# Optimization experiments

Measured on AMD Instinct MI355X. Metric: run time of the kernel, lower is better.

Reference implementation:

```python
import jax, jax.numpy as jnp
import numpy as np


def setup_inputs() -> dict:
    key = jax.random.key(0)
    ks = jax.random.split(key, 10)
    B, D_X, D_H, D_S, D_T = 16384, 256, 512, 128, 128
    G = 4 * D_H
    sc = lambda d: 1.0 / np.sqrt(d)
    return {
        "x": jax.random.normal(ks[0], (B, D_X), jnp.float32),
        "h": jax.random.normal(ks[1], (B, D_H), jnp.float32),
        "c": jax.random.normal(ks[2], (B, D_H), jnp.float32),
        "spatial_per_step": jax.random.normal(ks[3], (B, D_S), jnp.float32),
        "temporal_per_step": jax.random.normal(ks[4], (B, D_T), jnp.float32),
        "W_x": jax.random.normal(ks[5], (D_X, G), jnp.float32) * sc(D_X),
        "W_h": jax.random.normal(ks[6], (D_H, G), jnp.float32) * sc(D_H),
        "b_h": jax.random.normal(ks[7], (G,), jnp.float32) * 0.01,
        "W_s": jax.random.normal(ks[8], (D_S, G), jnp.float32) * sc(D_S),
        "W_t": jax.random.normal(ks[9], (D_T, G), jnp.float32) * sc(D_T),
    }


def reference(x, h, c, spatial_per_step, temporal_per_step, W_x, W_h, b_h, W_s, W_t):
    H = W_h.shape[0]  # hidden_size
    # Four gate projections summed (the fusion opportunity): [B, 4H]
    preact = (x @ W_x) + (h @ W_h + b_h) + (spatial_per_step @ W_s) + (temporal_per_step @ W_t)
    i_g = jax.nn.sigmoid(preact[:, 0 * H:1 * H])
    f_g = jax.nn.sigmoid(preact[:, 1 * H:2 * H])
    o_g = jax.nn.sigmoid(preact[:, 2 * H:3 * H])
    c_g = jnp.tanh(preact[:, 3 * H:4 * H])
    c_new = f_g * c + i_g * c_g
    # NOTE: faithful to the source, h = tanh(o * c) (not o * tanh(c))
    h_new = jnp.tanh(o_g * c_new)
    return (h_new, c_new)
```

## Files before the change

### kernel.cpp

```cpp
#include <hip/hip_runtime.h>
#include <hip/hip_bf16.h>
#include <cstdint>

#define B_DIM 16384
#define DX 256
#define DH 512
#define DS 128
#define DT 128
#define KDIM 1024
#define NDIM 2048
#define HOUT 512

typedef __attribute__((ext_vector_type(8))) short short8;
typedef __attribute__((ext_vector_type(4))) float floatx4;

union bf16x8 {
  short8 v;
  __hip_bfloat16 b[8];
};

__device__ __forceinline__ float fast_sigmoid(float x) {
  return 1.f / (1.f + __expf(-x));
}
__device__ __forceinline__ float fast_tanh(float x) {
  float e = __expf(-2.f * x);
  return (1.f - e) / (1.f + e);
}


__global__ __launch_bounds__(256) void pack_AW(
    const float* __restrict__ x, const float* __restrict__ h,
    const float* __restrict__ sp_, const float* __restrict__ tp_,
    const float* __restrict__ Wx, const float* __restrict__ Wh,
    const float* __restrict__ Ws, const float* __restrict__ Wt,
    __hip_bfloat16* __restrict__ Ap, __hip_bfloat16* __restrict__ Wp) {
  const int NA = B_DIM * KDIM / 8 / 256;
  const int bid = blockIdx.x;
  if (bid < NA) {
    int tid = bid * 256 + threadIdx.x;
    int i = tid & 63;
    int t32 = (tid >> 6) & 31;
    int tile = tid >> 11;
    int kb = tile & 15, mb = tile >> 4;
    int s = t32 >> 4, c = t32 & 15;
    int row = c * 16 + (i >> 2);
    int kq = (i & 3) ^ ((row >> 1) & 3);
    int b = mb * 256 + row;
    int k = kb * 64 + s * 32 + kq * 8;
    const float* p;
    if (k < 768) {
      p = (k < 256) ? (x + (size_t)b * DX + k) : (h + (size_t)b * DH + (k - 256));
    } else {
      p = (k < 896) ? (sp_ + (size_t)b * DS + (k - 768))
                    : (tp_ + (size_t)b * DT + (k - 896));
    }
    floatx4 v0 = *(const floatx4*)p;
    floatx4 v1 = *(const floatx4*)(p + 4);
    bf16x8 o;
#pragma unroll
    for (int j = 0; j < 4; ++j) {
      o.b[j]     = __float2bfloat16(v0[j]);
      o.b[4 + j] = __float2bfloat16(v1[j]);
    }
    *(short8*)(Ap + (size_t)tid * 8) = o.v;
  } else {
    int tid = (bid - NA) * 256 + threadIdx.x;
    int i = tid & 63;
    int t16 = (tid >> 6) & 15;
    int tile = tid >> 10;
    int kb = tile & 15, nblk = tile >> 4;
    int s = t16 >> 3, c = t16 & 7;
    int pcol = c * 16 + (i >> 2);
    int kq = (i & 3) ^ ((pcol >> 1) & 3);
    int k = kb * 64 + s * 32 + kq * 8;
    int wn = pcol >> 6, g = (pcol >> 4) & 3, hl = pcol & 15;
    int col = g * 512 + nblk * 32 + wn * 16 + hl;
    const float* src; int kl;
    if (k < 256)      { src = Wx; kl = k; }
    else if (k < 768) { src = Wh; kl = k - 256; }
    else if (k < 896) { src = Ws; kl = k - 768; }
    else              { src = Wt; kl = k - 896; }
    bf16x8 o;
#pragma unroll
    for (int r = 0; r < 8; ++r)
      o.b[r] = __float2bfloat16(src[(size_t)(kl + r) * NDIM + col]);
    *(short8*)(Wp + (size_t)tid * 8) = o.v;
  }
}

#define GLD(src, dst)                                              \
  __builtin_amdgcn_global_load_lds(                                \
      (const __attribute__((address_space(1))) void*)(src),        \
      (__attribute__((address_space(3))) void*)(dst), 16, 0, 0)

__global__ __launch_bounds__(256, 2) void lstm_gemm(
    const __hip_bfloat16* __restrict__ Ap, const __hip_bfloat16* __restrict__ Wp,
    const float* __restrict__ bh, const float* __restrict__ c_in,
    float* __restrict__ out) {
  __shared__ unsigned short As[16384];
  __shared__ unsigned short Bs[8192];

  const int tid = threadIdx.x;
  const int lane = tid & 63;
  const int wid = tid >> 6;
  const int wm = wid & 1;
  const int wn = wid >> 1;
  const int q = lane >> 4;
  const int fr = lane & 15;

  const int bid = blockIdx.x;
  const int wg = (bid & 7) * 128 + (bid >> 3);
  const int mb = wg >> 4;
  const int nblk = wg & 15;
  const int m0 = mb * 256;

  int aOff[8], bOff[4];
#pragma unroll
  for (int m = 0; m < 8; ++m) {
    int row = wm * 128 + m * 16 + fr;
    aOff[m] = row * 32 + (q ^ ((row >> 1) & 3)) * 8;
  }
#pragma unroll
  for (int n = 0; n < 4; ++n) {
    int colc = wn * 64 + n * 16 + fr;
    bOff[n] = colc * 32 + (q ^ ((colc >> 1) & 3)) * 8;
  }

  floatx4 acc[8][4];
#pragma unroll
  for (int i = 0; i < 8; ++i)
#pragma unroll
    for (int j = 0; j < 4; ++j) acc[i][j] = (floatx4)0.f;

  const __hip_bfloat16* aTile = Ap + (size_t)(mb * 16) * 16384 + lane * 8;
  const __hip_bfloat16* bTile = Wp + (size_t)(nblk * 16) * 8192 + lane * 8;

  for (int kb = 0; kb < 16; ++kb) {
    const __hip_bfloat16* ap = aTile + (size_t)kb * 16384;
    const __hip_bfloat16* bp = bTile + (size_t)kb * 8192;
#pragma unroll
    for (int j = 0; j < 8; ++j) {
      const int ca = wid * 8 + j;
      GLD(ap + ca * 512, &As[ca * 512]);
    }
#pragma unroll
    for (int j = 0; j < 4; ++j) {
      const int cb = wid * 4 + j;
      GLD(bp + cb * 512, &Bs[cb * 512]);
    }
    __syncthreads();

#pragma unroll
    for (int s = 0; s < 2; ++s) {
      short8 af[8], bf[4];
#pragma unroll
      for (int i = 0; i < 8; ++i)
        af[i] = *(const short8*)&As[s * 8192 + aOff[i]];
#pragma unroll
      for (int i = 0; i < 4; ++i)
        bf[i] = *(const short8*)&Bs[s * 4096 + bOff[i]];
#pragma unroll
      for (int mi = 0; mi < 8; ++mi)
#pragma unroll
        for (int ni = 0; ni < 4; ++ni)
          acc[mi][ni] = __builtin_amdgcn_mfma_f32_16x16x32_bf16(
              af[mi], bf[ni], acc[mi][ni], 0, 0, 0);
    }
    __syncthreads();
  }

  const int hh = nblk * 32 + wn * 16 + fr;
  float bias[4];
#pragma unroll
  for (int g = 0; g < 4; ++g) bias[g] = bh[g * 512 + hh];

#pragma unroll
  for (int mi = 0; mi < 8; ++mi) {
#pragma unroll
    for (int r = 0; r < 4; ++r) {
      const size_t grow = (size_t)(m0 + wm * 128 + mi * 16 + q * 4 + r);
      const float pi = acc[mi][0][r] + bias[0];
      const float pf = acc[mi][1][r] + bias[1];
      const float po = acc[mi][2][r] + bias[2];
      const float pc = acc[mi][3][r] + bias[3];
      const float ig = fast_sigmoid(pi);
      const float fg = fast_sigmoid(pf);
      const float og = fast_sigmoid(po);
      const float cg = fast_tanh(pc);
      const float cc = fg * c_in[grow * HOUT + hh] + ig * cg;
      out[grow * HOUT + hh] = fast_tanh(og * cc);
      out[(size_t)B_DIM * HOUT + grow * HOUT + hh] = cc;
    }
  }
}

extern "C" void kernel_launch(void* const* d_in, const int* in_sizes, int n_in,
                              void* d_out, int out_size, void* d_ws, size_t ws_size,
                              hipStream_t stream) {
  const float* x  = (const float*)d_in[0];
  const float* h  = (const float*)d_in[1];
  const float* c  = (const float*)d_in[2];
  const float* sp = (const float*)d_in[3];
  const float* tp = (const float*)d_in[4];
  const float* Wx = (const float*)d_in[5];
  const float* Wh = (const float*)d_in[6];
  const float* bh = (const float*)d_in[7];
  const float* Ws = (const float*)d_in[8];
  const float* Wt = (const float*)d_in[9];
  float* out = (float*)d_out;

  __hip_bfloat16* Ap = (__hip_bfloat16*)d_ws;
  __hip_bfloat16* Wp = (__hip_bfloat16*)((char*)d_ws + (size_t)B_DIM * KDIM * 2);

  const int nblk_A = B_DIM * KDIM / 8 / 256;
  const int nblk_W = NDIM * KDIM / 8 / 256;
  pack_AW<<<dim3(nblk_A + nblk_W), dim3(256), 0, stream>>>(
      x, h, sp, tp, Wx, Wh, Ws, Wt, Ap, Wp);
  lstm_gemm<<<dim3(1024), dim3(256), 0, stream>>>(Ap, Wp, bh, c, out);
}
```

Before: 238.5 us.

## Load MFMA fragments directly from global with register double-buffering, dropping LDS

Each wave in the GEMM now reads its bf16 A and B fragments straight from the pre-packed global buffers into registers. This replaces the global_load_lds staging into shared memory and the two __syncthreads per k-block. Two register fragment sets alternate, so the loads for the next k-slice are issued while MFMAs run on the current one. The XOR bank swizzle in the pack kernel is removed because LDS is no longer used. The cost is duplicate global/L1 traffic, since two waves now read the same A and B fragments, plus extra VGPR pressure from the double-buffered fragments.

```diff
diff --git a/kernel.cpp b/kernel.cpp
--- a/kernel.cpp
+++ b/kernel.cpp
@@ -44,7 +44,7 @@
     int kb = tile & 15, mb = tile >> 4;
     int s = t32 >> 4, c = t32 & 15;
     int row = c * 16 + (i >> 2);
-    int kq = (i & 3) ^ ((row >> 1) & 3);
+    int kq = i & 3;
     int b = mb * 256 + row;
     int k = kb * 64 + s * 32 + kq * 8;
     const float* p;
@@ -71,7 +71,7 @@
     int kb = tile & 15, nblk = tile >> 4;
     int s = t16 >> 3, c = t16 & 7;
     int pcol = c * 16 + (i >> 2);
-    int kq = (i & 3) ^ ((pcol >> 1) & 3);
+    int kq = i & 3;
     int k = kb * 64 + s * 32 + kq * 8;
     int wn = pcol >> 6, g = (pcol >> 4) & 3, hl = pcol & 15;
     int col = g * 512 + nblk * 32 + wn * 16 + hl;
@@ -88,18 +88,30 @@
   }
 }
 
-#define GLD(src, dst)                                              \
-  __builtin_amdgcn_global_load_lds(                                \
-      (const __attribute__((address_space(1))) void*)(src),        \
-      (__attribute__((address_space(3))) void*)(dst), 16, 0, 0)
+#define LOADP(Af, Bf, p) do {                                          \
+    const __hip_bfloat16* ap_ = aT + (size_t)(p) * 8192;               \
+    const __hip_bfloat16* bp_ = bT + (size_t)(p) * 4096;               \
+    _Pragma("unroll")                                                  \
+    for (int mi_ = 0; mi_ < 8; ++mi_)                                  \
+      Af[mi_] = *(const short8*)(ap_ + mi_ * 512);                     \
+    _Pragma("unroll")                                                  \
+    for (int ni_ = 0; ni_ < 4; ++ni_)                                  \
+      Bf[ni_] = *(const short8*)(bp_ + ni_ * 512);                     \
+  } while (0)
+
+#define MFMAP(Af, Bf) do {                                             \
+    _Pragma("unroll")                                                  \
+    for (int mi_ = 0; mi_ < 8; ++mi_)                                  \
+      _Pragma("unroll")                                                \
+      for (int ni_ = 0; ni_ < 4; ++ni_)                                \
+        acc[mi_][ni_] = __builtin_amdgcn_mfma_f32_16x16x32_bf16(       \
+            Af[mi_], Bf[ni_], acc[mi_][ni_], 0, 0, 0);                 \
+  } while (0)
 
 __global__ __launch_bounds__(256, 2) void lstm_gemm(
     const __hip_bfloat16* __restrict__ Ap, const __hip_bfloat16* __restrict__ Wp,
     const float* __restrict__ bh, const float* __restrict__ c_in,
     float* __restrict__ out) {
-  __shared__ unsigned short As[16384];
-  __shared__ unsigned short Bs[8192];
-
   const int tid = threadIdx.x;
   const int lane = tid & 63;
   const int wid = tid >> 6;
@@ -114,60 +126,29 @@
   const int nblk = wg & 15;
   const int m0 = mb * 256;
 
-  int aOff[8], bOff[4];
-#pragma unroll
-  for (int m = 0; m < 8; ++m) {
-    int row = wm * 128 + m * 16 + fr;
-    aOff[m] = row * 32 + (q ^ ((row >> 1) & 3)) * 8;
+  const int ls = (fr * 4 + q) * 8;
+  const __hip_bfloat16* aT =
+      Ap + (size_t)mb * 262144 + (wm * 8) * 512 + ls;
+  const __hip_bfloat16* bT =
+      Wp + (size_t)nblk * 131072 + (wn * 4) * 512 + ls;
+
+  floatx4 acc[8][4];
+#pragma unroll
+  for (int i = 0; i < 8; ++i)
+#pragma unroll
+    for (int j = 0; j < 4; ++j) acc[i][j] = (floatx4)0.f;
+
+  short8 aP[8], bP[4], aQ[8], bQ[4];
+  LOADP(aP, bP, 0);
+  for (int p = 0; p < 30; p += 2) {
+    LOADP(aQ, bQ, p + 1);
+    MFMAP(aP, bP);
+    LOADP(aP, bP, p + 2);
+    MFMAP(aQ, bQ);
   }
-#pragma unroll
-  for (int n = 0; n < 4; ++n) {
-    int colc = wn * 64 + n * 16 + fr;
-    bOff[n] = colc * 32 + (q ^ ((colc >> 1) & 3)) * 8;
-  }
-
-  floatx4 acc[8][4];
-#pragma unroll
-  for (int i = 0; i < 8; ++i)
-#pragma unroll
-    for (int j = 0; j < 4; ++j) acc[i][j] = (floatx4)0.f;
-
-  const __hip_bfloat16* aTile = Ap + (size_t)(mb * 16) * 16384 + lane * 8;
-  const __hip_bfloat16* bTile = Wp + (size_t)(nblk * 16) * 8192 + lane * 8;
-
-  for (int kb = 0; kb < 16; ++kb) {
-    const __hip_bfloat16* ap = aTile + (size_t)kb * 16384;
-    const __hip_bfloat16* bp = bTile + (size_t)kb * 8192;
-#pragma unroll
-    for (int j = 0; j < 8; ++j) {
-      const int ca = wid * 8 + j;
-      GLD(ap + ca * 512, &As[ca * 512]);
-    }
-#pragma unroll
-    for (int j = 0; j < 4; ++j) {
-      const int cb = wid * 4 + j;
-      GLD(bp + cb * 512, &Bs[cb * 512]);
-    }
-    __syncthreads();
-
-#pragma unroll
-    for (int s = 0; s < 2; ++s) {
-      short8 af[8], bf[4];
-#pragma unroll
-      for (int i = 0; i < 8; ++i)
-        af[i] = *(const short8*)&As[s * 8192 + aOff[i]];
-#pragma unroll
-      for (int i = 0; i < 4; ++i)
-        bf[i] = *(const short8*)&Bs[s * 4096 + bOff[i]];
-#pragma unroll
-      for (int mi = 0; mi < 8; ++mi)
-#pragma unroll
-        for (int ni = 0; ni < 4; ++ni)
-          acc[mi][ni] = __builtin_amdgcn_mfma_f32_16x16x32_bf16(
-              af[mi], bf[ni], acc[mi][ni], 0, 0, 0);
-    }
-    __syncthreads();
-  }
+  LOADP(aQ, bQ, 31);
+  MFMAP(aP, bP);
+  MFMAP(aQ, bQ);
 
   const int hh = nblk * 32 + wn * 16 + fr;
   float bias[4];
```

Result: slower. 272.1 us (+14.1%).

## Triple-buffer LDS pipeline with 512-thread 256x256 tiles for LSTM GEMM

Applied to the files above, without the earlier changes.

Enlarges each workgroup to 512 threads covering a 256x256 output tile (8 waves) and repacks the weights to 64-column blocks. The K loop is restructured into 32 half-steps with a three-stage LDS ring buffer in dynamic shared memory, issuing async global-to-LDS loads two steps ahead. Loads are interleaved with MFMA bursts and raised wave priority, and a single partial vmcnt wait plus barrier per step replaces the two full syncthreads. The goal is to hide global load latency and halve B-tile re-reads, at the cost of 96KB of LDS per block and more register pressure.

```diff
diff --git a/kernel.cpp b/kernel.cpp
--- a/kernel.cpp
+++ b/kernel.cpp
@@ -10,6 +10,9 @@
 #define KDIM 1024
 #define NDIM 2048
 #define HOUT 512
+
+#define NT 32
+#define PAN 8192
 
 typedef __attribute__((ext_vector_type(8))) short short8;
 typedef __attribute__((ext_vector_type(4))) float floatx4;
@@ -66,15 +69,15 @@
   } else {
     int tid = (bid - NA) * 256 + threadIdx.x;
     int i = tid & 63;
-    int t16 = (tid >> 6) & 15;
-    int tile = tid >> 10;
-    int kb = tile & 15, nblk = tile >> 4;
-    int s = t16 >> 3, c = t16 & 7;
+    int t32 = (tid >> 6) & 31;
+    int tile = tid >> 11;
+    int kb = tile & 15, nb = tile >> 4;
+    int s = t32 >> 4, c = t32 & 15;
     int pcol = c * 16 + (i >> 2);
     int kq = (i & 3) ^ ((pcol >> 1) & 3);
     int k = kb * 64 + s * 32 + kq * 8;
     int wn = pcol >> 6, g = (pcol >> 4) & 3, hl = pcol & 15;
-    int col = g * 512 + nblk * 32 + wn * 16 + hl;
+    int col = g * 512 + nb * 64 + wn * 16 + hl;
     const float* src; int kl;
     if (k < 256)      { src = Wx; kl = k; }
     else if (k < 768) { src = Wh; kl = k - 256; }
@@ -93,12 +96,13 @@
       (const __attribute__((address_space(1))) void*)(src),        \
       (__attribute__((address_space(3))) void*)(dst), 16, 0, 0)
 
-__global__ __launch_bounds__(256, 2) void lstm_gemm(
+__global__ __launch_bounds__(512, 2) void lstm_gemm(
     const __hip_bfloat16* __restrict__ Ap, const __hip_bfloat16* __restrict__ Wp,
     const float* __restrict__ bh, const float* __restrict__ c_in,
     float* __restrict__ out) {
-  __shared__ unsigned short As[16384];
-  __shared__ unsigned short Bs[8192];
+  extern __shared__ unsigned short smem[];
+  unsigned short* As = smem;
+  unsigned short* Bs = smem + 3 * PAN;
 
   const int tid = threadIdx.x;
   const int lane = tid & 63;
@@ -109,9 +113,9 @@
   const int fr = lane & 15;
 
   const int bid = blockIdx.x;
-  const int wg = (bid & 7) * 128 + (bid >> 3);
-  const int mb = wg >> 4;
-  const int nblk = wg & 15;
+  const int wg = (bid & 7) * 64 + (bid >> 3);
+  const int mb = wg >> 3;
+  const int nb = wg & 7;
   const int m0 = mb * 256;
 
   int aOff[8], bOff[4];
@@ -122,8 +126,8 @@
   }
 #pragma unroll
   for (int n = 0; n < 4; ++n) {
-    int colc = wn * 64 + n * 16 + fr;
-    bOff[n] = colc * 32 + (q ^ ((colc >> 1) & 3)) * 8;
+    int prow = wn * 64 + n * 16 + fr;
+    bOff[n] = prow * 32 + (q ^ ((prow >> 1) & 3)) * 8;
   }
 
   floatx4 acc[8][4];
@@ -132,44 +136,66 @@
 #pragma unroll
     for (int j = 0; j < 4; ++j) acc[i][j] = (floatx4)0.f;
 
-  const __hip_bfloat16* aTile = Ap + (size_t)(mb * 16) * 16384 + lane * 8;
-  const __hip_bfloat16* bTile = Wp + (size_t)(nblk * 16) * 8192 + lane * 8;
-
-  for (int kb = 0; kb < 16; ++kb) {
-    const __hip_bfloat16* ap = aTile + (size_t)kb * 16384;
-    const __hip_bfloat16* bp = bTile + (size_t)kb * 8192;
-#pragma unroll
-    for (int j = 0; j < 8; ++j) {
-      const int ca = wid * 8 + j;
-      GLD(ap + ca * 512, &As[ca * 512]);
-    }
-#pragma unroll
-    for (int j = 0; j < 4; ++j) {
-      const int cb = wid * 4 + j;
-      GLD(bp + cb * 512, &Bs[cb * 512]);
-    }
-    __syncthreads();
-
-#pragma unroll
-    for (int s = 0; s < 2; ++s) {
-      short8 af[8], bf[4];
-#pragma unroll
-      for (int i = 0; i < 8; ++i)
-        af[i] = *(const short8*)&As[s * 8192 + aOff[i]];
-#pragma unroll
-      for (int i = 0; i < 4; ++i)
-        bf[i] = *(const short8*)&Bs[s * 4096 + bOff[i]];
-#pragma unroll
-      for (int mi = 0; mi < 8; ++mi)
-#pragma unroll
-        for (int ni = 0; ni < 4; ++ni)
-          acc[mi][ni] = __builtin_amdgcn_mfma_f32_16x16x32_bf16(
-              af[mi], bf[ni], acc[mi][ni], 0, 0, 0);
-    }
-    __syncthreads();
-  }
-
-  const int hh = nblk * 32 + wn * 16 + fr;
+  const int ch0 = wid * 2;
+  const __hip_bfloat16* aStg = Ap + (size_t)mb * 262144 + ch0 * 512 + lane * 8;
+  const __hip_bfloat16* bStg = Wp + (size_t)nb * 262144 + ch0 * 512 + lane * 8;
+  const int dA = ch0 * 512;
+
+  GLD(aStg,              &As[dA]);        GLD(aStg + 512,        &As[dA + 512]);
+  GLD(bStg,              &Bs[dA]);        GLD(bStg + 512,        &Bs[dA + 512]);
+  GLD(aStg + 8192,       &As[PAN + dA]);  GLD(aStg + 8192 + 512, &As[PAN + dA + 512]);
+  GLD(bStg + 8192,       &Bs[PAN + dA]);  GLD(bStg + 8192 + 512, &Bs[PAN + dA + 512]);
+  asm volatile("s_waitcnt vmcnt(4)\n\ts_barrier" ::: "memory");
+
+  int sR = 0;
+  int sS = 2;
+
+  for (int t = 0; t < NT; ++t) {
+    const unsigned short* Ar = As + sR * PAN;
+    const unsigned short* Br = Bs + sR * PAN;
+    const int ts = (t + 2 < NT) ? (t + 2) : (NT - 1);
+    const __hip_bfloat16* aP = aStg + (size_t)ts * PAN;
+    const __hip_bfloat16* bP = bStg + (size_t)ts * PAN;
+    unsigned short* Aw = As + sS * PAN;
+    unsigned short* Bw = Bs + sS * PAN;
+
+    short8 a0[4], bf[4];
+#pragma unroll
+    for (int i = 0; i < 4; ++i) a0[i] = *(const short8*)(Ar + aOff[i]);
+#pragma unroll
+    for (int i = 0; i < 4; ++i) bf[i] = *(const short8*)(Br + bOff[i]);
+    GLD(aP, &Aw[dA]);
+    GLD(aP + 512, &Aw[dA + 512]);
+    __builtin_amdgcn_s_setprio(1);
+#pragma unroll
+    for (int mi = 0; mi < 4; ++mi)
+#pragma unroll
+      for (int ni = 0; ni < 4; ++ni)
+        acc[mi][ni] = __builtin_amdgcn_mfma_f32_16x16x32_bf16(
+            a0[mi], bf[ni], acc[mi][ni], 0, 0, 0);
+    __builtin_amdgcn_s_setprio(0);
+
+    short8 a1[4];
+#pragma unroll
+    for (int i = 0; i < 4; ++i) a1[i] = *(const short8*)(Ar + aOff[4 + i]);
+    GLD(bP, &Bw[dA]);
+    GLD(bP + 512, &Bw[dA + 512]);
+    __builtin_amdgcn_s_setprio(1);
+#pragma unroll
+    for (int mi = 0; mi < 4; ++mi)
+#pragma unroll
+      for (int ni = 0; ni < 4; ++ni)
+        acc[4 + mi][ni] = __builtin_amdgcn_mfma_f32_16x16x32_bf16(
+            a1[mi], bf[ni], acc[4 + mi][ni], 0, 0, 0);
+    __builtin_amdgcn_s_setprio(0);
+
+    asm volatile("s_waitcnt vmcnt(4)\n\ts_barrier" ::: "memory");
+
+    sR = (sR == 2) ? 0 : sR + 1;
+    sS = (sS == 2) ? 0 : sS + 1;
+  }
+
+  const int hh = nb * 64 + wn * 16 + fr;
   float bias[4];
 #pragma unroll
   for (int g = 0; g < 4; ++g) bias[g] = bh[g * 512 + hh];
@@ -212,9 +238,16 @@
   __hip_bfloat16* Ap = (__hip_bfloat16*)d_ws;
   __hip_bfloat16* Wp = (__hip_bfloat16*)((char*)d_ws + (size_t)B_DIM * KDIM * 2);
 
+  static bool attr_done = false;
+  if (!attr_done) {
+    hipFuncSetAttribute((const void*)lstm_gemm,
+                        hipFuncAttributeMaxDynamicSharedMemorySize, 98304);
+    attr_done = true;
+  }
+
   const int nblk_A = B_DIM * KDIM / 8 / 256;
   const int nblk_W = NDIM * KDIM / 8 / 256;
   pack_AW<<<dim3(nblk_A + nblk_W), dim3(256), 0, stream>>>(
       x, h, sp, tp, Wx, Wh, Ws, Wt, Ap, Wp);
-  lstm_gemm<<<dim3(1024), dim3(256), 0, stream>>>(Ap, Wp, bh, c, out);
-}
+  lstm_gemm<<<dim3(512), dim3(512), 98304, stream>>>(Ap, Wp, bh, c, out);
+}
```

New measurement: 231.6 us. 2.9% less time.
